# Kernel optimization log

Measured on AMD Instinct MI355X. Metric: run time of the kernel, lower is better.

Reference implementation:

```python
import jax, jax.numpy as jnp
import numpy as np

B, F, ND, H, H1, M, NSEL = 8192, 40, 10, 64, 16, 75, 60
GRU_L = 3


def setup_inputs() -> dict:
    key = jax.random.key(0)
    ks = iter(jax.random.split(key, 64))
    def nrm(shape, scale=1.0):
        return jax.random.normal(next(ks), shape, jnp.float32) * scale
    d = {}
    d["X"] = nrm((B, 22, F))
    d["A"] = jax.random.uniform(next(ks), (B, 22, 22), dtype=jnp.float32)
    FO = F + (F - ND)  # 70: tiled R features + node-specific features
    for br, fin in (("R", F), ("O", FO), ("D", FO)):
        d[f"Wg_{br}"] = nrm((fin, H), fin ** -0.5)
        d[f"bg_{br}"] = jnp.zeros((H,), jnp.float32)
    for br, gin in (("R", 2 * H), ("O", 3 * H), ("D", 2 * H)):
        d[f"Wz_{br}"] = nrm((gin, H), gin ** -0.5)
        d[f"Wr_{br}"] = nrm((gin, H), gin ** -0.5)
        d[f"Wm_{br}"] = nrm((gin, H), gin ** -0.5)
        d[f"bm_{br}"] = jnp.zeros((H,), jnp.float32)
    for br in "ROD":
        d[f"W1_{br}"] = nrm((H, H1), H ** -0.5)
        d[f"b1_{br}"] = jnp.zeros((H1,), jnp.float32)
        d[f"W2_{br}"] = nrm((H1, 1), H1 ** -0.5)
    # temporal branch: 3 role-specific learned season vectors + fwd/bwd 1-unit GRUs
    d["temporal"] = nrm((3, M), 0.1)
    d["gru_k"] = nrm((3, 2, 3))      # [branch, fwd/bwd, (z,r,h)] input kernels (input dim 1)
    d["gru_rk"] = nrm((3, 2, 3))     # recurrent kernels (units=1)
    d["gru_b"] = jnp.zeros((3, 2, 2, 3), jnp.float32)  # reset_after=True: input & recurrent bias
    d["wout"] = nrm((3,))            # output Dense(1, no bias) on 1-dim GRU output
    d["ys_succ_ind"] = jnp.sort(jax.random.randint(next(ks), (NSEL,), 0, M))
    return d


def _temporal_probs(t, k, rk, b, wo, idx):
    # t:[M]  k,rk:[2,3]  b:[2,2,3]  wo: scalar. Keras GRU (units=1, reset_after=True).
    def make_step(kk, rkk, bb):
        def step(h, x):
            z = jax.nn.sigmoid(x * kk[0] + bb[0, 0] + h * rkk[0] + bb[1, 0])
            r = jax.nn.sigmoid(x * kk[1] + bb[0, 1] + h * rkk[1] + bb[1, 1])
            hh = jnp.tanh(x * kk[2] + bb[0, 2] + r * (h * rkk[2] + bb[1, 2]))
            hn = z * h + (1.0 - z) * hh
            return hn, hn
        return step
    h0 = jnp.zeros((), t.dtype)
    _, f = jax.lax.scan(make_step(k[0], rk[0], b[0]), h0, t)          # forward GRU
    _, g = jax.lax.scan(make_step(k[1], rk[1], b[1]), h0, f[::-1])     # go_backwards GRU (keeps reversed order, as Keras)
    p = jax.nn.softmax(g * wo)   # softmax over M time steps
    return p[idx]                # gather successful-season indices -> [NSEL]


def _fwd(X, A, Wg_R, bg_R, Wg_O, bg_O, Wg_D, bg_D,
         Wz_R, Wr_R, Wm_R, bm_R, Wz_O, Wr_O, Wm_O, bm_O,
         Wz_D, Wr_D, Wm_D, bm_D,
         W1_R, b1_R, W2_R, W1_O, b1_O, W2_O, W1_D, b1_D, W2_D,
         temporal, gru_k, gru_rk, gru_b, wout, ys_succ_ind):
    X_R = X[:, :1, :]                                               # [B,1,F]
    X_O = jnp.concatenate([jnp.tile(X_R, (1, 10, 1)), X[:, 1:11, ND:]], -1)  # [B,10,FO]
    X_D = jnp.concatenate([jnp.tile(X_R, (1, 11, 1)), X[:, 11:, ND:]], -1)   # [B,11,FO]
    A_RO = A[:, :1, 1:11]    # R <- O  [B,1,10]
    A_OR = A[:, 1:11, :1]    # O <- R  [B,10,1]
    A_OD = A[:, 1:11, 11:]   # O <- D  [B,10,11]
    A_DO = A[:, 11:, 1:11]   # D <- O  [B,11,10]
    h_R = jnp.tanh(X_R @ Wg_R + bg_R)
    h_O = jnp.tanh(X_O @ Wg_O + bg_O)
    h_D = jnp.tanh(X_D @ Wg_D + bg_D)
    def gate(h, n, Wz, Wr, Wm, bm):
        hn = jnp.concatenate([h, n], -1)
        z = jax.nn.sigmoid(hn @ Wz)
        r = jax.nn.sigmoid(hn @ Wr)
        hm = jnp.tanh(jnp.concatenate([h * r, n], -1) @ Wm + bm)
        return (1.0 - z) * h + z * hm
    for _ in range(GRU_L):
        n_R = A_RO @ h_O                                            # [B,1,H]
        n_O = jnp.concatenate([A_OR @ h_R, A_OD @ h_D], -1)         # [B,10,2H]
        n_D = A_DO @ h_O                                            # [B,11,H]
        h_R = gate(h_R, n_R, Wz_R, Wr_R, Wm_R, bm_R)
        h_O = gate(h_O, n_O, Wz_O, Wr_O, Wm_O, bm_O)
        h_D = gate(h_D, n_D, Wz_D, Wr_D, Wm_D, bm_D)
    s_R = (jnp.tanh(h_R @ W1_R + b1_R) @ W2_R)[:, 0]                # squeeze node dim -> [B,1]
    s_O = jnp.sum(jnp.tanh(h_O @ W1_O + b1_O) @ W2_O, axis=1)       # [B,1]
    s_D = jnp.sum(jnp.tanh(h_D @ W1_D + b1_D) @ W2_D, axis=1)       # [B,1]
    tp = jax.vmap(_temporal_probs, in_axes=(0, 0, 0, 0, 0, None))(
        temporal, gru_k, gru_rk, gru_b, wout, ys_succ_ind)          # [3,NSEL]
    return s_R * tp[0] + s_O * tp[1] + s_D * tp[2]                  # [B,NSEL]


def reference(X, A, Wg_R, bg_R, Wg_O, bg_O, Wg_D, bg_D,
              Wz_R, Wr_R, Wm_R, bm_R, Wz_O, Wr_O, Wm_O, bm_O,
              Wz_D, Wr_D, Wm_D, bm_D,
              W1_R, b1_R, W2_R, W1_O, b1_O, W2_O, W1_D, b1_D, W2_D,
              temporal, gru_k, gru_rk, gru_b, wout, ys_succ_ind):
    return _fwd(X, A, Wg_R, bg_R, Wg_O, bg_O, Wg_D, bg_D,
                Wz_R, Wr_R, Wm_R, bm_R, Wz_O, Wr_O, Wm_O, bm_O,
                Wz_D, Wr_D, Wm_D, bm_D,
                W1_R, b1_R, W2_R, W1_O, b1_O, W2_O, W1_D, b1_D, W2_D,
                temporal, gru_k, gru_rk, gru_b, wout, ys_succ_ind)
```

## Files before the change

### kernel.cpp

```cpp
#include <hip/hip_runtime.h>
#include <hip/hip_bf16.h>
#include <math.h>

#define DEV __device__ __forceinline__

DEV float sigmoidf_(float x) { return 1.0f / (1.0f + __expf(-x)); }

#define R10(OP) OP(0) OP(1) OP(2) OP(3) OP(4) OP(5) OP(6) OP(7) OP(8) OP(9)
#define R11(OP) R10(OP) OP(10)

#define AROB 0
#define AORB 16
#define AODB 32
#define ADOB 144
#define ANUM 256

#define DOT_ARO() (sA2[AROB+0]*hO0 + sA2[AROB+1]*hO1 + sA2[AROB+2]*hO2 + sA2[AROB+3]*hO3 \
                 + sA2[AROB+4]*hO4 + sA2[AROB+5]*hO5 + sA2[AROB+6]*hO6 + sA2[AROB+7]*hO7 \
                 + sA2[AROB+8]*hO8 + sA2[AROB+9]*hO9)
#define DOT_AOD(i) (sA2[AODB+(i)*11+0]*hD0 + sA2[AODB+(i)*11+1]*hD1 + sA2[AODB+(i)*11+2]*hD2 \
                  + sA2[AODB+(i)*11+3]*hD3 + sA2[AODB+(i)*11+4]*hD4 + sA2[AODB+(i)*11+5]*hD5 \
                  + sA2[AODB+(i)*11+6]*hD6 + sA2[AODB+(i)*11+7]*hD7 + sA2[AODB+(i)*11+8]*hD8 \
                  + sA2[AODB+(i)*11+9]*hD9 + sA2[AODB+(i)*11+10]*hD10)
#define DOT_ADO(i) (sA2[ADOB+(i)*10+0]*hO0 + sA2[ADOB+(i)*10+1]*hO1 + sA2[ADOB+(i)*10+2]*hO2 \
                  + sA2[ADOB+(i)*10+3]*hO3 + sA2[ADOB+(i)*10+4]*hO4 + sA2[ADOB+(i)*10+5]*hO5 \
                  + sA2[ADOB+(i)*10+6]*hO6 + sA2[ADOB+(i)*10+7]*hO7 + sA2[ADOB+(i)*10+8]*hO8 \
                  + sA2[ADOB+(i)*10+9]*hO9)

DEV float gstep(float x, float h, const float* k, const float* rk, const float* bb) {
  const float z  = sigmoidf_(fmaf(x, k[0], bb[0]) + fmaf(h, rk[0], bb[3]));
  const float r  = sigmoidf_(fmaf(x, k[1], bb[1]) + fmaf(h, rk[1], bb[4]));
  const float hh = tanhf(fmaf(x, k[2], bb[2]) + r * fmaf(h, rk[2], bb[5]));
  return z * h + (1.f - z) * hh;
}

__global__ void __launch_bounds__(64, 1)
temporal_kernel(const float* __restrict__ T, const float* __restrict__ GK,
                const float* __restrict__ GRK, const float* __restrict__ GB,
                const float* __restrict__ WO, const int* __restrict__ IDX,
                float* __restrict__ tp) {
  const int i = threadIdx.x;
  __shared__ float fb[3][75];
  __shared__ float gg[3][75];
  if (i < 3) {
    float k0[3], k1[3], rk0[3], rk1[3];
#pragma unroll
    for (int q = 0; q < 3; ++q) {
      k0[q]  = GK[i * 6 + q];      k1[q]  = GK[i * 6 + 3 + q];
      rk0[q] = GRK[i * 6 + q];     rk1[q] = GRK[i * 6 + 3 + q];
    }
    const float* B0 = GB + i * 12;
    const float* B1 = GB + i * 12 + 6;
    float h = 0.f;
    for (int s = 0; s < 75; ++s) { h = gstep(T[i * 75 + s], h, k0, rk0, B0); fb[i][s] = h; }
    h = 0.f;
    for (int s = 0; s < 75; ++s) { h = gstep(fb[i][74 - s], h, k1, rk1, B1); gg[i][s] = h; }
    const float wo = WO[i];
    float mx = -1e30f;
    for (int s = 0; s < 75; ++s) mx = fmaxf(mx, gg[i][s] * wo);
    float sum = 0.f;
    for (int s = 0; s < 75; ++s) { const float e = __expf(gg[i][s] * wo - mx); fb[i][s] = e; sum += e; }
    const float inv = 1.f / sum;
    for (int j = 0; j < 60; ++j) tp[i * 60 + j] = fb[i][IDX[j]] * inv;
  }
}

__global__ void __launch_bounds__(256)
__attribute__((amdgpu_waves_per_eu(4, 4)))
ggnn_main(
    const float* __restrict__ X, const float* __restrict__ A,
    const float* __restrict__ WgR, const float* __restrict__ bgR,
    const float* __restrict__ WgO, const float* __restrict__ bgO,
    const float* __restrict__ WgD, const float* __restrict__ bgD,
    const float* __restrict__ WzR, const float* __restrict__ WrR,
    const float* __restrict__ WmR, const float* __restrict__ bmR,
    const float* __restrict__ WzO, const float* __restrict__ WrO,
    const float* __restrict__ WmO, const float* __restrict__ bmO,
    const float* __restrict__ WzD, const float* __restrict__ WrD,
    const float* __restrict__ WmD, const float* __restrict__ bmD,
    const float* __restrict__ W1R, const float* __restrict__ b1R, const float* __restrict__ W2R,
    const float* __restrict__ W1O, const float* __restrict__ b1O, const float* __restrict__ W2O,
    const float* __restrict__ W1D, const float* __restrict__ b1D, const float* __restrict__ W2D,
    const float* __restrict__ tp, int B, float* __restrict__ out) {
  const int w = threadIdx.x >> 6;
  const int c = threadIdx.x & 63;
  const int b = blockIdx.x * 4 + w;

  __shared__ __align__(16) float smemAll[4 * 1920];
  __shared__ float sAAll[4 * ANUM];
  float* sm = smemAll + w * 1920;
  const float* sA2 = sAAll + w * ANUM;

  if (b >= B) return;

  const float* Xb = X + (size_t)b * 880;
  const float* Ab = A + (size_t)b * 484;
  for (int t = c; t < 880; t += 64) sm[t] = Xb[t];
  {
    float* sw = sAAll + w * ANUM;
    if (c < 10) {
      sw[AROB + c] = Ab[1 + c];
      sw[AORB + c] = Ab[(1 + c) * 22];
    }
    for (int t = c; t < 110; t += 64) {
      const int i = t / 11, j = t - i * 11;
      sw[AODB + t] = Ab[(1 + i) * 22 + 11 + j];
    }
    for (int t = c; t < 110; t += 64) {
      const int i = t / 10, j = t - i * 10;
      sw[ADOB + t] = Ab[(11 + i) * 22 + 1 + j];
    }
  }

  float hR;
#define DECLHO(i) float hO##i;
  R10(DECLHO)
#undef DECLHO
#define DECLHD(i) float hD##i;
  R11(DECLHD)
#undef DECLHD
  {
    float aR = bgR[c], cO = bgO[c], cD = bgD[c];
#pragma unroll 4
    for (int k = 0; k < 40; ++k) {
      const float x = sm[k];
      aR = fmaf(x, WgR[k * 64 + c], aR);
      cO = fmaf(x, WgO[k * 64 + c], cO);
      cD = fmaf(x, WgD[k * 64 + c], cD);
    }
    hR = tanhf(aR);
#define DECLAO(i) float aO##i = cO;
    R10(DECLAO)
#undef DECLAO
#define DECLAD(i) float aD##i = cD;
    R11(DECLAD)
#undef DECLAD
#pragma unroll 2
    for (int k = 0; k < 30; ++k) {
      const float wo_ = WgO[(40 + k) * 64 + c];
      const float wd_ = WgD[(40 + k) * 64 + c];
#define AOSTEP(i) aO##i = fmaf(sm[(1 + i) * 40 + 10 + k], wo_, aO##i);
      R10(AOSTEP)
#undef AOSTEP
#define ADSTEP(i) aD##i = fmaf(sm[(11 + i) * 40 + 10 + k], wd_, aD##i);
      R11(ADSTEP)
#undef ADSTEP
    }
#define TANHO(i) hO##i = tanhf(aO##i);
    R10(TANHO)
#undef TANHO
#define TANHD(i) hD##i = tanhf(aD##i);
    R11(TANHD)
#undef TANHD
  }

  for (int it = 0; it < 3; ++it) {
    const float nR = DOT_ARO();
#define DECLND(i) const float nD##i = DOT_ADO(i);
    R11(DECLND)
#undef DECLND

#define STAGEO(i) sm[i * 192 + c] = hO##i; \
                  sm[i * 192 + 64 + c] = sA2[AORB + i] * hR; \
                  sm[i * 192 + 128 + c] = DOT_AOD(i);
    R10(STAGEO)
#undef STAGEO
    {
#define DECLZR(i) float az##i = 0.f, ar##i = 0.f;
      R10(DECLZR)
#undef DECLZR
#pragma unroll 2
      for (int k4 = 0; k4 < 192; k4 += 4) {
        const float wa0 = WzO[(k4 + 0) * 64 + c], wa1 = WzO[(k4 + 1) * 64 + c];
        const float wa2 = WzO[(k4 + 2) * 64 + c], wa3 = WzO[(k4 + 3) * 64 + c];
        const float wb0 = WrO[(k4 + 0) * 64 + c], wb1 = WrO[(k4 + 1) * 64 + c];
        const float wb2 = WrO[(k4 + 2) * 64 + c], wb3 = WrO[(k4 + 3) * 64 + c];
#define MSTEP(i) { const float4 v = *reinterpret_cast<const float4*>(&sm[i * 192 + k4]); \
        az##i = fmaf(v.x, wa0, az##i); az##i = fmaf(v.y, wa1, az##i); \
        az##i = fmaf(v.z, wa2, az##i); az##i = fmaf(v.w, wa3, az##i); \
        ar##i = fmaf(v.x, wb0, ar##i); ar##i = fmaf(v.y, wb1, ar##i); \
        ar##i = fmaf(v.z, wb2, ar##i); ar##i = fmaf(v.w, wb3, ar##i); }
        R10(MSTEP)
#undef MSTEP
      }
#define SIGZR(i) const float z##i = sigmoidf_(az##i); const float r##i = sigmoidf_(ar##i);
      R10(SIGZR)
#undef SIGZR
#define STAGEHR(i) sm[i * 192 + c] = hO##i * r##i;
      R10(STAGEHR)
#undef STAGEHR
#define DECLAM(i) float am##i = bmO[c];
      R10(DECLAM)
#undef DECLAM
#pragma unroll 2
      for (int k4 = 0; k4 < 192; k4 += 4) {
        const float w0 = WmO[(k4 + 0) * 64 + c], w1 = WmO[(k4 + 1) * 64 + c];
        const float w2 = WmO[(k4 + 2) * 64 + c], w3 = WmO[(k4 + 3) * 64 + c];
#define MSTEP(i) { const float4 v = *reinterpret_cast<const float4*>(&sm[i * 192 + k4]); \
        am##i = fmaf(v.x, w0, am##i); am##i = fmaf(v.y, w1, am##i); \
        am##i = fmaf(v.z, w2, am##i); am##i = fmaf(v.w, w3, am##i); }
        R10(MSTEP)
#undef MSTEP
      }
#define UPDO(i) hO##i = (1.f - z##i) * hO##i + z##i * tanhf(am##i);
      R10(UPDO)
#undef UPDO
    }

#define STAGEDD(i) sm[i * 128 + c] = hD##i; \
                   sm[i * 128 + 64 + c] = nD##i;
    R11(STAGEDD)
#undef STAGEDD
    sm[1408 + c] = hR;
    sm[1472 + c] = nR;
    {
#define DECLZR(i) float az##i = 0.f, ar##i = 0.f;
      R11(DECLZR)
#undef DECLZR
      float azR = 0.f, arR = 0.f;
#pragma unroll 2
      for (int k4 = 0; k4 < 128; k4 += 4) {
        const float wa0 = WzD[(k4 + 0) * 64 + c], wa1 = WzD[(k4 + 1) * 64 + c];
        const float wa2 = WzD[(k4 + 2) * 64 + c], wa3 = WzD[(k4 + 3) * 64 + c];
        const float wb0 = WrD[(k4 + 0) * 64 + c], wb1 = WrD[(k4 + 1) * 64 + c];
        const float wb2 = WrD[(k4 + 2) * 64 + c], wb3 = WrD[(k4 + 3) * 64 + c];
#define MSTEP(i) { const float4 v = *reinterpret_cast<const float4*>(&sm[i * 128 + k4]); \
        az##i = fmaf(v.x, wa0, az##i); az##i = fmaf(v.y, wa1, az##i); \
        az##i = fmaf(v.z, wa2, az##i); az##i = fmaf(v.w, wa3, az##i); \
        ar##i = fmaf(v.x, wb0, ar##i); ar##i = fmaf(v.y, wb1, ar##i); \
        ar##i = fmaf(v.z, wb2, ar##i); ar##i = fmaf(v.w, wb3, ar##i); }
        R11(MSTEP)
#undef MSTEP
        const float wza0 = WzR[(k4 + 0) * 64 + c], wza1 = WzR[(k4 + 1) * 64 + c];
        const float wza2 = WzR[(k4 + 2) * 64 + c], wza3 = WzR[(k4 + 3) * 64 + c];
        const float wra0 = WrR[(k4 + 0) * 64 + c], wra1 = WrR[(k4 + 1) * 64 + c];
        const float wra2 = WrR[(k4 + 2) * 64 + c], wra3 = WrR[(k4 + 3) * 64 + c];
        const float4 vr = *reinterpret_cast<const float4*>(&sm[1408 + k4]);
        azR = fmaf(vr.x, wza0, azR); azR = fmaf(vr.y, wza1, azR);
        azR = fmaf(vr.z, wza2, azR); azR = fmaf(vr.w, wza3, azR);
        arR = fmaf(vr.x, wra0, arR); arR = fmaf(vr.y, wra1, arR);
        arR = fmaf(vr.z, wra2, arR); arR = fmaf(vr.w, wra3, arR);
      }
#define SIGZR(i) const float z##i = sigmoidf_(az##i); const float r##i = sigmoidf_(ar##i);
      R11(SIGZR)
#undef SIGZR
      const float zR_ = sigmoidf_(azR);
      const float rR_ = sigmoidf_(arR);
#define STAGEHR(i) sm[i * 128 + c] = hD##i * r##i;
      R11(STAGEHR)
#undef STAGEHR
      sm[1408 + c] = hR * rR_;
#define DECLAM(i) float am##i = bmD[c];
      R11(DECLAM)
#undef DECLAM
      float amR = bmR[c];
#pragma unroll 2
      for (int k4 = 0; k4 < 128; k4 += 4) {
        const float w0 = WmD[(k4 + 0) * 64 + c], w1 = WmD[(k4 + 1) * 64 + c];
        const float w2 = WmD[(k4 + 2) * 64 + c], w3 = WmD[(k4 + 3) * 64 + c];
#define MSTEP(i) { const float4 v = *reinterpret_cast<const float4*>(&sm[i * 128 + k4]); \
        am##i = fmaf(v.x, w0, am##i); am##i = fmaf(v.y, w1, am##i); \
        am##i = fmaf(v.z, w2, am##i); am##i = fmaf(v.w, w3, am##i); }
        R11(MSTEP)
#undef MSTEP
        const float wm0 = WmR[(k4 + 0) * 64 + c], wm1 = WmR[(k4 + 1) * 64 + c];
        const float wm2 = WmR[(k4 + 2) * 64 + c], wm3 = WmR[(k4 + 3) * 64 + c];
        const float4 vr = *reinterpret_cast<const float4*>(&sm[1408 + k4]);
        amR = fmaf(vr.x, wm0, amR); amR = fmaf(vr.y, wm1, amR);
        amR = fmaf(vr.z, wm2, amR); amR = fmaf(vr.w, wm3, amR);
      }
#define UPDD(i) hD##i = (1.f - z##i) * hD##i + z##i * tanhf(am##i);
      R11(UPDD)
#undef UPDD
      hR = (1.f - zR_) * hR + zR_ * tanhf(amR);
    }
  }

  sm[c] = hR;
#define STASH_O(i) sm[(1 + i) * 64 + c] = hO##i;
  R10(STASH_O)
#undef STASH_O
#define STASH_D(i) sm[(11 + i) * 64 + c] = hD##i;
  R11(STASH_D)
#undef STASH_D

  const int g = c >> 4;
  const int c1 = c & 15;
  float pR = 0.f, pO = 0.f, pD = 0.f;
  for (int rr = g; rr < 22; rr += 4) {
    const float* W1; const float* b1; const float* W2;
    if (rr == 0)      { W1 = W1R; b1 = b1R; W2 = W2R; }
    else if (rr < 11) { W1 = W1O; b1 = b1O; W2 = W2O; }
    else              { W1 = W1D; b1 = b1D; W2 = W2D; }
    float a = b1[c1];
#pragma unroll 8
    for (int kk = 0; kk < 64; ++kk) {
      const int k = (kk + (g << 4)) & 63;
      a = fmaf(sm[rr * 64 + k], W1[k * 16 + c1], a);
    }
    const float t = tanhf(a) * W2[c1];
    if (rr == 0) pR += t;
    else if (rr < 11) pO += t;
    else pD += t;
  }
#pragma unroll
  for (int off = 32; off >= 1; off >>= 1) {
    pR += __shfl_xor(pR, off, 64);
    pO += __shfl_xor(pO, off, 64);
    pD += __shfl_xor(pD, off, 64);
  }
  if (c < 60) {
    out[(size_t)b * 60 + c] = pR * tp[c] + pO * tp[60 + c] + pD * tp[120 + c];
  }
}

extern "C" void kernel_launch(void* const* d_in, const int* in_sizes, int n_in,
                              void* d_out, int out_size, void* d_ws, size_t ws_size,
                              hipStream_t stream) {
  const float* X   = (const float*)d_in[0];
  const float* A   = (const float*)d_in[1];
  const float* WgR = (const float*)d_in[2];
  const float* bgR = (const float*)d_in[3];
  const float* WgO = (const float*)d_in[4];
  const float* bgO = (const float*)d_in[5];
  const float* WgD = (const float*)d_in[6];
  const float* bgD = (const float*)d_in[7];
  const float* WzR = (const float*)d_in[8];
  const float* WrR = (const float*)d_in[9];
  const float* WmR = (const float*)d_in[10];
  const float* bmR = (const float*)d_in[11];
  const float* WzO = (const float*)d_in[12];
  const float* WrO = (const float*)d_in[13];
  const float* WmO = (const float*)d_in[14];
  const float* bmO = (const float*)d_in[15];
  const float* WzD = (const float*)d_in[16];
  const float* WrD = (const float*)d_in[17];
  const float* WmD = (const float*)d_in[18];
  const float* bmD = (const float*)d_in[19];
  const float* W1R = (const float*)d_in[20];
  const float* b1R = (const float*)d_in[21];
  const float* W2R = (const float*)d_in[22];
  const float* W1O = (const float*)d_in[23];
  const float* b1O = (const float*)d_in[24];
  const float* W2O = (const float*)d_in[25];
  const float* W1D = (const float*)d_in[26];
  const float* b1D = (const float*)d_in[27];
  const float* W2D = (const float*)d_in[28];
  const float* Tmp = (const float*)d_in[29];
  const float* GK  = (const float*)d_in[30];
  const float* GRK = (const float*)d_in[31];
  const float* GB  = (const float*)d_in[32];
  const float* WO  = (const float*)d_in[33];
  const int*   IDX = (const int*)d_in[34];

  float* tp = (float*)d_ws;
  const int B = in_sizes[0] / 880;

  hipLaunchKernelGGL(temporal_kernel, dim3(1), dim3(64), 0, stream, Tmp, GK, GRK, GB, WO, IDX, tp);
  hipLaunchKernelGGL(ggnn_main, dim3((B + 3) / 4), dim3(256), 0, stream,
                     X, A, WgR, bgR, WgO, bgO, WgD, bgD,
                     WzR, WrR, WmR, bmR, WzO, WrO, WmO, bmO, WzD, WrD, WmD, bmD,
                     W1R, b1R, W2R, W1O, b1O, W2O, W1D, b1D, W2D,
                     tp, B, (float*)d_out);
}
```

Before: 1.003 ms.

## Split GRU gate matmuls into node halves to cut registers and double occupancy

Splits the O-branch and D-branch GRU gate matmuls into two passes over node halves (5+5 and 6+5). This lowers the number of live accumulators per thread, and the launch bounds change from waves_per_eu(4,4) to launch_bounds(256,2) to allow more resident waves. The D and R updates are decoupled, and neighbour sums go to a separate shared-memory region, so LDS per wave grows from 1920 to 2752 floats. In exchange, each weight matrix is reloaded from global/L2 twice per iteration, and the z/r loops are no longer unrolled.

After: 1.234 ms. +23.0%, slower.

```diff
diff --git a/kernel.cpp b/kernel.cpp
--- a/kernel.cpp
+++ b/kernel.cpp
@@ -8,6 +8,10 @@
 
 #define R10(OP) OP(0) OP(1) OP(2) OP(3) OP(4) OP(5) OP(6) OP(7) OP(8) OP(9)
 #define R11(OP) R10(OP) OP(10)
+#define R5A(OP) OP(0) OP(1) OP(2) OP(3) OP(4)
+#define R5B(OP) OP(5) OP(6) OP(7) OP(8) OP(9)
+#define R6A(OP) OP(0) OP(1) OP(2) OP(3) OP(4) OP(5)
+#define R5D(OP) OP(6) OP(7) OP(8) OP(9) OP(10)
 
 #define AROB 0
 #define AORB 16
@@ -26,6 +30,10 @@
                   + sA2[ADOB+(i)*10+3]*hO3 + sA2[ADOB+(i)*10+4]*hO4 + sA2[ADOB+(i)*10+5]*hO5 \
                   + sA2[ADOB+(i)*10+6]*hO6 + sA2[ADOB+(i)*10+7]*hO7 + sA2[ADOB+(i)*10+8]*hO8 \
                   + sA2[ADOB+(i)*10+9]*hO9)
+
+#define NDS 1920
+#define RS 2624
+#define SLICE 2752
 
 DEV float gstep(float x, float h, const float* k, const float* rk, const float* bb) {
   const float z  = sigmoidf_(fmaf(x, k[0], bb[0]) + fmaf(h, rk[0], bb[3]));
@@ -65,9 +73,7 @@
   }
 }
 
-__global__ void __launch_bounds__(256)
-__attribute__((amdgpu_waves_per_eu(4, 4)))
-ggnn_main(
+__global__ void __launch_bounds__(256, 2) ggnn_main(
     const float* __restrict__ X, const float* __restrict__ A,
     const float* __restrict__ WgR, const float* __restrict__ bgR,
     const float* __restrict__ WgO, const float* __restrict__ bgO,
@@ -86,9 +92,9 @@
   const int c = threadIdx.x & 63;
   const int b = blockIdx.x * 4 + w;
 
-  __shared__ __align__(16) float smemAll[4 * 1920];
+  __shared__ __align__(16) float smemAll[4 * SLICE];
   __shared__ float sAAll[4 * ANUM];
-  float* sm = smemAll + w * 1920;
+  float* sm = smemAll + w * SLICE;
   const float* sA2 = sAAll + w * ANUM;
 
   if (b >= B) return;
@@ -154,127 +160,157 @@
 #undef TANHD
   }
 
+  const float bmOc = bmO[c], bmDc = bmD[c], bmRc = bmR[c];
+
+#define OZDECL(i) float az##i = 0.f, ar##i = 0.f;
+#define OZST(i) { const float4 v = *reinterpret_cast<const float4*>(&sm[(i) * 192 + k4]); \
+    az##i = fmaf(v.x, wa0, az##i); az##i = fmaf(v.y, wa1, az##i); \
+    az##i = fmaf(v.z, wa2, az##i); az##i = fmaf(v.w, wa3, az##i); \
+    ar##i = fmaf(v.x, wb0, ar##i); ar##i = fmaf(v.y, wb1, ar##i); \
+    ar##i = fmaf(v.z, wb2, ar##i); ar##i = fmaf(v.w, wb3, ar##i); }
+#define OSIG(i) const float z##i = sigmoidf_(az##i); const float r##i = sigmoidf_(ar##i);
+#define OSTG(i) sm[(i) * 192 + c] = hO##i * r##i;
+#define OAMD(i) float am##i = bmOc;
+#define OMST(i) { const float4 v = *reinterpret_cast<const float4*>(&sm[(i) * 192 + k4]); \
+    am##i = fmaf(v.x, w0, am##i); am##i = fmaf(v.y, w1, am##i); \
+    am##i = fmaf(v.z, w2, am##i); am##i = fmaf(v.w, w3, am##i); }
+#define OUPD(i) hO##i = (1.f - z##i) * hO##i + z##i * tanhf(am##i);
+
+#define DZDECL(i) float az##i = 0.f, ar##i = 0.f;
+#define DZH(i) { const float4 v = *reinterpret_cast<const float4*>(&sm[(i) * 64 + k4]); \
+    az##i = fmaf(v.x, wa0, az##i); az##i = fmaf(v.y, wa1, az##i); \
+    az##i = fmaf(v.z, wa2, az##i); az##i = fmaf(v.w, wa3, az##i); \
+    ar##i = fmaf(v.x, wb0, ar##i); ar##i = fmaf(v.y, wb1, ar##i); \
+    ar##i = fmaf(v.z, wb2, ar##i); ar##i = fmaf(v.w, wb3, ar##i); }
+#define DZN(i) { const float4 v = *reinterpret_cast<const float4*>(&sm[NDS + (i) * 64 + k4]); \
+    az##i = fmaf(v.x, wa0, az##i); az##i = fmaf(v.y, wa1, az##i); \
+    az##i = fmaf(v.z, wa2, az##i); az##i = fmaf(v.w, wa3, az##i); \
+    ar##i = fmaf(v.x, wb0, ar##i); ar##i = fmaf(v.y, wb1, ar##i); \
+    ar##i = fmaf(v.z, wb2, ar##i); ar##i = fmaf(v.w, wb3, ar##i); }
+#define DSIG(i) const float z##i = sigmoidf_(az##i); const float r##i = sigmoidf_(ar##i);
+#define DSTG(i) sm[(i) * 64 + c] = hD##i * r##i;
+#define DAMD(i) float am##i = bmDc;
+#define DMH(i) { const float4 v = *reinterpret_cast<const float4*>(&sm[(i) * 64 + k4]); \
+    am##i = fmaf(v.x, w0, am##i); am##i = fmaf(v.y, w1, am##i); \
+    am##i = fmaf(v.z, w2, am##i); am##i = fmaf(v.w, w3, am##i); }
+#define DMN(i) { const float4 v = *reinterpret_cast<const float4*>(&sm[NDS + (i) * 64 + k4]); \
+    am##i = fmaf(v.x, w0, am##i); am##i = fmaf(v.y, w1, am##i); \
+    am##i = fmaf(v.z, w2, am##i); am##i = fmaf(v.w, w3, am##i); }
+#define DUPD(i) hD##i = (1.f - z##i) * hD##i + z##i * tanhf(am##i);
+
+#define LOADW_ZR(W1_, W2_, OFS) \
+    const float wa0 = W1_[(OFS + k4 + 0) * 64 + c], wa1 = W1_[(OFS + k4 + 1) * 64 + c]; \
+    const float wa2 = W1_[(OFS + k4 + 2) * 64 + c], wa3 = W1_[(OFS + k4 + 3) * 64 + c]; \
+    const float wb0 = W2_[(OFS + k4 + 0) * 64 + c], wb1 = W2_[(OFS + k4 + 1) * 64 + c]; \
+    const float wb2 = W2_[(OFS + k4 + 2) * 64 + c], wb3 = W2_[(OFS + k4 + 3) * 64 + c];
+#define LOADW_M(W_, OFS) \
+    const float w0 = W_[(OFS + k4 + 0) * 64 + c], w1 = W_[(OFS + k4 + 1) * 64 + c]; \
+    const float w2 = W_[(OFS + k4 + 2) * 64 + c], w3 = W_[(OFS + k4 + 3) * 64 + c];
+
   for (int it = 0; it < 3; ++it) {
-    const float nR = DOT_ARO();
-#define DECLND(i) const float nD##i = DOT_ADO(i);
-    R11(DECLND)
-#undef DECLND
-
+    sm[RS + c] = hR;
+    sm[RS + 64 + c] = DOT_ARO();
+#define SGND(i) sm[NDS + i * 64 + c] = DOT_ADO(i);
+    R11(SGND)
+#undef SGND
 #define STAGEO(i) sm[i * 192 + c] = hO##i; \
                   sm[i * 192 + 64 + c] = sA2[AORB + i] * hR; \
                   sm[i * 192 + 128 + c] = DOT_AOD(i);
     R10(STAGEO)
 #undef STAGEO
+
     {
-#define DECLZR(i) float az##i = 0.f, ar##i = 0.f;
-      R10(DECLZR)
-#undef DECLZR
-#pragma unroll 2
-      for (int k4 = 0; k4 < 192; k4 += 4) {
-        const float wa0 = WzO[(k4 + 0) * 64 + c], wa1 = WzO[(k4 + 1) * 64 + c];
-        const float wa2 = WzO[(k4 + 2) * 64 + c], wa3 = WzO[(k4 + 3) * 64 + c];
-        const float wb0 = WrO[(k4 + 0) * 64 + c], wb1 = WrO[(k4 + 1) * 64 + c];
-        const float wb2 = WrO[(k4 + 2) * 64 + c], wb3 = WrO[(k4 + 3) * 64 + c];
-#define MSTEP(i) { const float4 v = *reinterpret_cast<const float4*>(&sm[i * 192 + k4]); \
-        az##i = fmaf(v.x, wa0, az##i); az##i = fmaf(v.y, wa1, az##i); \
-        az##i = fmaf(v.z, wa2, az##i); az##i = fmaf(v.w, wa3, az##i); \
-        ar##i = fmaf(v.x, wb0, ar##i); ar##i = fmaf(v.y, wb1, ar##i); \
-        ar##i = fmaf(v.z, wb2, ar##i); ar##i = fmaf(v.w, wb3, ar##i); }
-        R10(MSTEP)
-#undef MSTEP
+      R5A(OZDECL)
+#pragma unroll 1
+      for (int k4 = 0; k4 < 192; k4 += 4) { LOADW_ZR(WzO, WrO, 0) R5A(OZST) }
+      R5A(OSIG) R5A(OSTG) R5A(OAMD)
+#pragma unroll 2
+      for (int k4 = 0; k4 < 192; k4 += 4) { LOADW_M(WmO, 0) R5A(OMST) }
+      R5A(OUPD)
+    }
+    {
+      R5B(OZDECL)
+#pragma unroll 1
+      for (int k4 = 0; k4 < 192; k4 += 4) { LOADW_ZR(WzO, WrO, 0) R5B(OZST) }
+      R5B(OSIG) R5B(OSTG) R5B(OAMD)
+#pragma unroll 2
+      for (int k4 = 0; k4 < 192; k4 += 4) { LOADW_M(WmO, 0) R5B(OMST) }
+      R5B(OUPD)
+    }
+
+#define SGHD(i) sm[i * 64 + c] = hD##i;
+    R11(SGHD)
+#undef SGHD
+
+    {
+      R6A(DZDECL)
+#pragma unroll 1
+      for (int k4 = 0; k4 < 64; k4 += 4) { LOADW_ZR(WzD, WrD, 0) R6A(DZH) }
+#pragma unroll 1
+      for (int k4 = 0; k4 < 64; k4 += 4) { LOADW_ZR(WzD, WrD, 64) R6A(DZN) }
+      R6A(DSIG) R6A(DSTG) R6A(DAMD)
+#pragma unroll 2
+      for (int k4 = 0; k4 < 64; k4 += 4) { LOADW_M(WmD, 0) R6A(DMH) }
+#pragma unroll 2
+      for (int k4 = 0; k4 < 64; k4 += 4) { LOADW_M(WmD, 64) R6A(DMN) }
+      R6A(DUPD)
+    }
+    {
+      R5D(DZDECL)
+#pragma unroll 1
+      for (int k4 = 0; k4 < 64; k4 += 4) { LOADW_ZR(WzD, WrD, 0) R5D(DZH) }
+#pragma unroll 1
+      for (int k4 = 0; k4 < 64; k4 += 4) { LOADW_ZR(WzD, WrD, 64) R5D(DZN) }
+      R5D(DSIG) R5D(DSTG) R5D(DAMD)
+#pragma unroll 2
+      for (int k4 = 0; k4 < 64; k4 += 4) { LOADW_M(WmD, 0) R5D(DMH) }
+#pragma unroll 2
+      for (int k4 = 0; k4 < 64; k4 += 4) { LOADW_M(WmD, 64) R5D(DMN) }
+      R5D(DUPD)
+    }
+
+    {
+      float azR = 0.f, arR = 0.f;
+#pragma unroll 2
+      for (int k4 = 0; k4 < 128; k4 += 4) {
+        LOADW_ZR(WzR, WrR, 0)
+        const float4 v = *reinterpret_cast<const float4*>(&sm[RS + k4]);
+        azR = fmaf(v.x, wa0, azR); azR = fmaf(v.y, wa1, azR);
+        azR = fmaf(v.z, wa2, azR); azR = fmaf(v.w, wa3, azR);
+        arR = fmaf(v.x, wb0, arR); arR = fmaf(v.y, wb1, arR);
+        arR = fmaf(v.z, wb2, arR); arR = fmaf(v.w, wb3, arR);
       }
-#define SIGZR(i) const float z##i = sigmoidf_(az##i); const float r##i = sigmoidf_(ar##i);
-      R10(SIGZR)
-#undef SIGZR
-#define STAGEHR(i) sm[i * 192 + c] = hO##i * r##i;
-      R10(STAGEHR)
-#undef STAGEHR
-#define DECLAM(i) float am##i = bmO[c];
-      R10(DECLAM)
-#undef DECLAM
-#pragma unroll 2
-      for (int k4 = 0; k4 < 192; k4 += 4) {
-        const float w0 = WmO[(k4 + 0) * 64 + c], w1 = WmO[(k4 + 1) * 64 + c];
-        const float w2 = WmO[(k4 + 2) * 64 + c], w3 = WmO[(k4 + 3) * 64 + c];
-#define MSTEP(i) { const float4 v = *reinterpret_cast<const float4*>(&sm[i * 192 + k4]); \
-        am##i = fmaf(v.x, w0, am##i); am##i = fmaf(v.y, w1, am##i); \
-        am##i = fmaf(v.z, w2, am##i); am##i = fmaf(v.w, w3, am##i); }
-        R10(MSTEP)
-#undef MSTEP
-      }
-#define UPDO(i) hO##i = (1.f - z##i) * hO##i + z##i * tanhf(am##i);
-      R10(UPDO)
-#undef UPDO
-    }
-
-#define STAGEDD(i) sm[i * 128 + c] = hD##i; \
-                   sm[i * 128 + 64 + c] = nD##i;
-    R11(STAGEDD)
-#undef STAGEDD
-    sm[1408 + c] = hR;
-    sm[1472 + c] = nR;
-    {
-#define DECLZR(i) float az##i = 0.f, ar##i = 0.f;
-      R11(DECLZR)
-#undef DECLZR
-      float azR = 0.f, arR = 0.f;
-#pragma unroll 2
-      for (int k4 = 0; k4 < 128; k4 += 4) {
-        const float wa0 = WzD[(k4 + 0) * 64 + c], wa1 = WzD[(k4 + 1) * 64 + c];
-        const float wa2 = WzD[(k4 + 2) * 64 + c], wa3 = WzD[(k4 + 3) * 64 + c];
-        const float wb0 = WrD[(k4 + 0) * 64 + c], wb1 = WrD[(k4 + 1) * 64 + c];
-        const float wb2 = WrD[(k4 + 2) * 64 + c], wb3 = WrD[(k4 + 3) * 64 + c];
-#define MSTEP(i) { const float4 v = *reinterpret_cast<const float4*>(&sm[i * 128 + k4]); \
-        az##i = fmaf(v.x, wa0, az##i); az##i = fmaf(v.y, wa1, az##i); \
-        az##i = fmaf(v.z, wa2, az##i); az##i = fmaf(v.w, wa3, az##i); \
-        ar##i = fmaf(v.x, wb0, ar##i); ar##i = fmaf(v.y, wb1, ar##i); \
-        ar##i = fmaf(v.z, wb2, ar##i); ar##i = fmaf(v.w, wb3, ar##i); }
-        R11(MSTEP)
-#undef MSTEP
-        const float wza0 = WzR[(k4 + 0) * 64 + c], wza1 = WzR[(k4 + 1) * 64 + c];
-        const float wza2 = WzR[(k4 + 2) * 64 + c], wza3 = WzR[(k4 + 3) * 64 + c];
-        const float wra0 = WrR[(k4 + 0) * 64 + c], wra1 = WrR[(k4 + 1) * 64 + c];
-        const float wra2 = WrR[(k4 + 2) * 64 + c], wra3 = WrR[(k4 + 3) * 64 + c];
-        const float4 vr = *reinterpret_cast<const float4*>(&sm[1408 + k4]);
-        azR = fmaf(vr.x, wza0, azR); azR = fmaf(vr.y, wza1, azR);
-        azR = fmaf(vr.z, wza2, azR); azR = fmaf(vr.w, wza3, azR);
-        arR = fmaf(vr.x, wra0, arR); arR = fmaf(vr.y, wra1, arR);
-        arR = fmaf(vr.z, wra2, arR); arR = fmaf(vr.w, wra3, arR);
-      }
-#define SIGZR(i) const float z##i = sigmoidf_(az##i); const float r##i = sigmoidf_(ar##i);
-      R11(SIGZR)
-#undef SIGZR
       const float zR_ = sigmoidf_(azR);
       const float rR_ = sigmoidf_(arR);
-#define STAGEHR(i) sm[i * 128 + c] = hD##i * r##i;
-      R11(STAGEHR)
-#undef STAGEHR
-      sm[1408 + c] = hR * rR_;
-#define DECLAM(i) float am##i = bmD[c];
-      R11(DECLAM)
-#undef DECLAM
-      float amR = bmR[c];
+      sm[RS + c] = hR * rR_;
+      float amR = bmRc;
 #pragma unroll 2
       for (int k4 = 0; k4 < 128; k4 += 4) {
-        const float w0 = WmD[(k4 + 0) * 64 + c], w1 = WmD[(k4 + 1) * 64 + c];
-        const float w2 = WmD[(k4 + 2) * 64 + c], w3 = WmD[(k4 + 3) * 64 + c];
-#define MSTEP(i) { const float4 v = *reinterpret_cast<const float4*>(&sm[i * 128 + k4]); \
-        am##i = fmaf(v.x, w0, am##i); am##i = fmaf(v.y, w1, am##i); \
-        am##i = fmaf(v.z, w2, am##i); am##i = fmaf(v.w, w3, am##i); }
-        R11(MSTEP)
-#undef MSTEP
-        const float wm0 = WmR[(k4 + 0) * 64 + c], wm1 = WmR[(k4 + 1) * 64 + c];
-        const float wm2 = WmR[(k4 + 2) * 64 + c], wm3 = WmR[(k4 + 3) * 64 + c];
-        const float4 vr = *reinterpret_cast<const float4*>(&sm[1408 + k4]);
-        amR = fmaf(vr.x, wm0, amR); amR = fmaf(vr.y, wm1, amR);
-        amR = fmaf(vr.z, wm2, amR); amR = fmaf(vr.w, wm3, amR);
+        LOADW_M(WmR, 0)
+        const float4 v = *reinterpret_cast<const float4*>(&sm[RS + k4]);
+        amR = fmaf(v.x, w0, amR); amR = fmaf(v.y, w1, amR);
+        amR = fmaf(v.z, w2, amR); amR = fmaf(v.w, w3, amR);
       }
-#define UPDD(i) hD##i = (1.f - z##i) * hD##i + z##i * tanhf(am##i);
-      R11(UPDD)
-#undef UPDD
       hR = (1.f - zR_) * hR + zR_ * tanhf(amR);
     }
   }
+
+#undef OZDECL
+#undef OZST
+#undef OSIG
+#undef OSTG
+#undef OAMD
+#undef OMST
+#undef OUPD
+#undef DZDECL
+#undef DZH
+#undef DZN
+#undef DSIG
+#undef DSTG
+#undef DAMD
+#undef DMH
+#undef DMN
+#undef DUPD
 
   sm[c] = hR;
 #define STASH_O(i) sm[(1 + i) * 64 + c] = hO##i;
```
